# Optimization experiments

Hardware: AMD Instinct MI355X
Metric: run time of the kernel (lower is better)

The kernel has to match this reference:

```python
import jax, jax.numpy as jnp
import numpy as np

SIGMA = 0.01        # config['fscore_sigma']
FSCORE_W = 0.1      # config['fscore_weight']
TASK_W = 1.0        # config['task_weight']
DOMAIN_W = 0.1      # config['domain_weight']


def setup_inputs() -> dict:
    key = jax.random.key(0)
    ks = jax.random.split(key, 11)
    B, N, M, F = 8, 4096, 4096, 512
    H1, H2, D = 256, 128, 6
    return {
        "pred_pc": jax.random.normal(ks[0], (B, N, 3), jnp.float32),
        "target_pc": jax.random.normal(ks[1], (B, M, 3), jnp.float32),
        "domain_features": jax.random.normal(ks[2], (B, F), jnp.float32),
        "dataset_weights": jax.random.uniform(ks[3], (B,), jnp.float32, 0.9, 1.2),
        "W1": jax.random.normal(ks[4], (F, H1), jnp.float32) * 0.02,
        "b1": jnp.zeros((H1,), jnp.float32),
        "W2": jax.random.normal(ks[5], (H1, H2), jnp.float32) * 0.02,
        "b2": jnp.zeros((H2,), jnp.float32),
        "W3": jax.random.normal(ks[6], (H2, D), jnp.float32) * 0.02,
        "b3": jnp.zeros((D,), jnp.float32),
        "domain_labels": jax.random.randint(ks[7], (B,), 0, D),
    }


def _chamfer_mins(pred, tgt):
    # pred: [B,N,3], tgt: [B,M,3] -> squared pairwise dists [B,N,M], then dual mins
    d = (jnp.sum(pred ** 2, axis=2)[:, :, None]
         + jnp.sum(tgt ** 2, axis=2)[:, None, :]
         - 2.0 * jnp.einsum('bnd,bmd->bnm', pred, tgt))
    return jnp.min(d, axis=2), jnp.min(d, axis=1)   # [B,N], [B,M]


def reference(pred_pc, target_pc, domain_features, dataset_weights,
              W1, b1, W2, b2, W3, b3, domain_labels):
    min_a, min_b = _chamfer_mins(pred_pc, target_pc)
    c = 2.0 * SIGMA * SIGMA
    soft_a = jnp.exp(-min_a / c)
    soft_b = jnp.exp(-min_b / c)

    # batch-level task loss (compute_reconstruction_loss on full batch)
    chamfer = jnp.mean(min_a) + jnp.mean(min_b)
    prec = jnp.mean(soft_a)
    rec = jnp.mean(soft_b)
    fscore = 2.0 * prec * rec / (prec + rec + 1e-8)
    task = chamfer + FSCORE_W * (1.0 - fscore)

    # per-sample dataset-weighted loss (vectorized form of the Python loop)
    ch_i = jnp.mean(min_a, axis=1) + jnp.mean(min_b, axis=1)
    p_i = jnp.mean(soft_a, axis=1)
    r_i = jnp.mean(soft_b, axis=1)
    f_i = 2.0 * p_i * r_i / (p_i + r_i + 1e-8)
    loss_i = ch_i + FSCORE_W * (1.0 - f_i)
    dataset_weighted = jnp.mean(dataset_weights * loss_i)

    # domain loss: GRL is identity in forward; classifier in eval mode (dropout off)
    h = jax.nn.relu(domain_features @ W1 + b1)
    h = jax.nn.relu(h @ W2 + b2)
    logits = h @ W3 + b3
    logp = jax.nn.log_softmax(logits, axis=-1)
    domain = -jnp.mean(jnp.take_along_axis(logp, domain_labels[:, None], axis=1))

    total = TASK_W * task + DOMAIN_W * domain + dataset_weighted
    return total
```

## Files before the change

kernel.cpp:

```cpp
#include <hip/hip_runtime.h>
#include <math.h>

#define B 8
#define NPTS 4096
#define QPT 8
#define THREADS 256

typedef float v2f __attribute__((ext_vector_type(2)));
typedef float v4f __attribute__((ext_vector_type(4)));

__device__ __forceinline__ float min3f(float a, float b, float c) {
  return fminf(fminf(a, b), c);
}

#if __has_builtin(__builtin_elementwise_fma)
__device__ __forceinline__ v2f fma2(v2f a, v2f b, v2f c) {
  return __builtin_elementwise_fma(a, b, c);
}
#else
__device__ __forceinline__ v2f fma2(v2f a, v2f b, v2f c) {
  v2f r; r.x = __builtin_fmaf(a.x, b.x, c.x); r.y = __builtin_fmaf(a.y, b.y, c.y);
  return r;
}
#endif

#define VLO(v) __builtin_shufflevector(v, v, 0, 1)
#define VHI(v) __builtin_shufflevector(v, v, 2, 3)


template<int S, int LOG2S>
__global__ __launch_bounds__(THREADS, 4) void k1_kernel(
    const float* __restrict__ pred, const float* __restrict__ targ,
    const float* __restrict__ x, const float* __restrict__ W1,
    float* __restrict__ partial, float* __restrict__ sums64,
    float* __restrict__ h1p) {
  constexpr int REFS = NPTS / S;
  const int tid = threadIdx.x;
  const int cid = blockIdx.x;

  __shared__ __align__(16) float sx[REFS];
  __shared__ __align__(16) float sy[REFS];
  __shared__ __align__(16) float sz[REFS];
  __shared__ __align__(16) float sw[REFS];
  __shared__ float xs[64];

  if (cid < 64) {
    if (cid == 0 && tid < 64) sums64[tid] = 0.f;
    int b = cid >> 3, kc = cid & 7;
    if (tid < 64) xs[tid] = x[b * 512 + kc * 64 + tid];
    __syncthreads();
    float acc = 0.f;
    const float* w = W1 + (size_t)(kc * 64) * 256 + tid;
#pragma unroll 8
    for (int k = 0; k < 64; ++k) acc = fmaf(xs[k], w[k * 256], acc);
    h1p[(b * 8 + kc) * 256 + tid] = acc;
  }

  int split  = cid & (S - 1);
  int qchunk = (cid >> LOG2S) & 1;
  int b      = (cid >> (LOG2S + 1)) & 7;
  int dir    = cid >> (LOG2S + 4);
  const float* qp = dir ? targ : pred;
  const float* rp = dir ? pred : targ;

  const float* rb = rp + ((size_t)b * NPTS + (size_t)split * REFS) * 3;
  for (int i = tid; i < REFS; i += THREADS) {
    float xx = rb[i * 3 + 0], yy = rb[i * 3 + 1], zz = rb[i * 3 + 2];
    sx[i] = xx; sy[i] = yy; sz[i] = zz;
    sw[i] = 0.5f * (xx * xx + yy * yy + zz * zz);
  }
  __syncthreads();

  const float* qb = qp + (size_t)b * NPTS * 3;
  int q0 = qchunk * (QPT * THREADS) + tid;
  float qx[QPT], qy[QPT], qz[QPT], vmin[QPT];
#pragma unroll
  for (int i = 0; i < QPT; ++i) {
    int q = q0 + i * THREADS;
    qx[i] = qb[q * 3 + 0];
    qy[i] = qb[q * 3 + 1];
    qz[i] = qb[q * 3 + 2];
    vmin[i] = 3.4e38f;
  }

  for (int j = 0; j < REFS; j += 8) {
    v4f xA = *(const v4f*)(sx + j), xB = *(const v4f*)(sx + j + 4);
    v4f yA = *(const v4f*)(sy + j), yB = *(const v4f*)(sy + j + 4);
    v4f zA = *(const v4f*)(sz + j), zB = *(const v4f*)(sz + j + 4);
    v4f wA = *(const v4f*)(sw + j), wB = *(const v4f*)(sw + j + 4);
    v2f x01 = VLO(xA), x23 = VHI(xA), x45 = VLO(xB), x67 = VHI(xB);
    v2f y01 = VLO(yA), y23 = VHI(yA), y45 = VLO(yB), y67 = VHI(yB);
    v2f z01 = VLO(zA), z23 = VHI(zA), z45 = VLO(zB), z67 = VHI(zB);
    v2f w01 = VLO(wA), w23 = VHI(wA), w45 = VLO(wB), w67 = VHI(wB);
#pragma unroll
    for (int i = 0; i < QPT; ++i) {
      v2f nx = {-qx[i], -qx[i]};
      v2f ny = {-qy[i], -qy[i]};
      v2f nz = {-qz[i], -qz[i]};
      v2f s01 = fma2(nx, x01, fma2(ny, y01, fma2(nz, z01, w01)));
      v2f s23 = fma2(nx, x23, fma2(ny, y23, fma2(nz, z23, w23)));
      v2f s45 = fma2(nx, x45, fma2(ny, y45, fma2(nz, z45, w45)));
      v2f s67 = fma2(nx, x67, fma2(ny, y67, fma2(nz, z67, w67)));
      float m0 = min3f(s01.x, s01.y, s23.x);
      float m1 = min3f(s23.y, s45.x, s45.y);
      float m2 = min3f(s67.x, s67.y, m0);
      vmin[i] = min3f(m1, m2, vmin[i]);
    }
  }

  size_t base = (((size_t)dir * B + b) * S + split) * NPTS;
#pragma unroll
  for (int i = 0; i < QPT; ++i) {
    float qn = fmaf(qx[i], qx[i], fmaf(qy[i], qy[i], qz[i] * qz[i]));
    partial[base + q0 + i * THREADS] = fmaf(2.f, vmin[i], qn);
  }
}

template<int S>
__global__ __launch_bounds__(THREADS) void k2_kernel(
    const float* __restrict__ partial, float* __restrict__ sums64,
    const float* __restrict__ h1p, const float* __restrict__ b1,
    const float* __restrict__ W2, const float* __restrict__ b2,
    const float* __restrict__ W3, const float* __restrict__ b3,
    const int* __restrict__ labels, const float* __restrict__ wgt,
    float* __restrict__ out) {
  const int id = blockIdx.x;
  const int tid = threadIdx.x;
  __shared__ float red[8];
  __shared__ bool is_last;

  int chunk = id & 15;
  int b   = (id >> 4) & 7;
  int dir = id >> 7;
  size_t pb = ((size_t)dir * B + b) * S * NPTS;
  int q = chunk * 256 + tid;

  float m = 3.4e38f;
#pragma unroll
  for (int s = 0; s < S; ++s)
    m = fminf(m, partial[pb + (size_t)s * NPTS + q]);
  float s_min = m;
  float s_soft = __expf(-5000.0f * m);

  for (int off = 32; off > 0; off >>= 1) {
    s_min  += __shfl_down(s_min,  off);
    s_soft += __shfl_down(s_soft, off);
  }
  int wave = tid >> 6, lane = tid & 63;
  if (lane == 0) { red[wave * 2] = s_min; red[wave * 2 + 1] = s_soft; }
  __syncthreads();
  if (tid == 0) {
    float a = 0.f, c = 0.f;
    for (int wv = 0; wv < 4; ++wv) { a += red[wv * 2]; c += red[wv * 2 + 1]; }
    atomicAdd(&sums64[(dir * B + b) * 2 + 0], a);
    atomicAdd(&sums64[(dir * B + b) * 2 + 1], c);
    __threadfence();
    unsigned t = atomicAdd((unsigned*)(sums64 + 32), 1u);
    is_last = (t == 255u);
  }
  __syncthreads();
  if (!is_last) return;
  __threadfence();

  __shared__ float h1s[8 * 256];
  __shared__ float h2s[8 * 128];
  __shared__ float lg[48];
  __shared__ float nlls[8];

  for (int i = tid; i < 2048; i += THREADS) {
    int bb = i >> 8, k = i & 255;
    float a = b1[k];
#pragma unroll
    for (int p = 0; p < 8; ++p) a += h1p[(bb * 8 + p) * 256 + k];
    h1s[i] = fmaxf(a, 0.f);
  }
  __syncthreads();
  for (int i = tid; i < 1024; i += THREADS) {
    int bb = i >> 7, jo = i & 127;
    float acc = b2[jo];
    const float* w2 = W2 + jo;
    const float* h1r = h1s + bb * 256;
#pragma unroll 8
    for (int k = 0; k < 256; ++k) acc = fmaf(h1r[k], w2[(size_t)k * 128], acc);
    h2s[i] = fmaxf(acc, 0.f);
  }
  __syncthreads();
  if (tid < 48) {
    int bb = tid / 6, d = tid % 6;
    float acc = b3[d];
#pragma unroll 8
    for (int k = 0; k < 128; ++k)
      acc = fmaf(h2s[bb * 128 + k], W3[k * 6 + d], acc);
    lg[tid] = acc;
  }
  __syncthreads();
  if (tid < 8) {
    int bb = tid;
    float mx = lg[bb * 6];
    for (int d = 1; d < 6; ++d) mx = fmaxf(mx, lg[bb * 6 + d]);
    float se = 0.f;
    for (int d = 0; d < 6; ++d) se += __expf(lg[bb * 6 + d] - mx);
    int lab = labels[bb];
    nlls[bb] = -(lg[bb * 6 + lab] - mx - __logf(se));
  }
  __syncthreads();
  if (tid == 0) {
    volatile const float* vs = (volatile const float*)sums64;
    float chamfer = 0.f, prec = 0.f, rec = 0.f, dsw = 0.f, dom = 0.f;
    for (int bb = 0; bb < B; ++bb) {
      float sa  = vs[(0 * B + bb) * 2 + 0];
      float ssa = vs[(0 * B + bb) * 2 + 1];
      float sb  = vs[(1 * B + bb) * 2 + 0];
      float ssb = vs[(1 * B + bb) * 2 + 1];
      float ma = sa / 4096.f, mb = sb / 4096.f;
      float p = ssa / 4096.f, r = ssb / 4096.f;
      chamfer += ma + mb;
      prec += p; rec += r;
      float f_i = 2.f * p * r / (p + r + 1e-8f);
      float loss_i = ma + mb + 0.1f * (1.f - f_i);
      dsw += wgt[bb] * loss_i;
      dom += nlls[bb];
    }
    chamfer *= (1.f / B); prec *= (1.f / B); rec *= (1.f / B);
    dsw *= (1.f / B); dom *= (1.f / B);
    float fscore = 2.f * prec * rec / (prec + rec + 1e-8f);
    float task = chamfer + 0.1f * (1.f - fscore);
    out[0] = 1.0f * task + 0.1f * dom + dsw;
  }
}

template<int S, int LOG2S>
static void run_pipeline(const float* pred, const float* targ, const float* x,
                         const float* wgt, const float* W1, const float* b1,
                         const float* W2, const float* b2, const float* W3,
                         const float* b3, const int* labels, float* out,
                         char* ws, hipStream_t stream) {
  float* partial = (float*)ws;
  float* sums64  = partial + (size_t)2 * B * S * NPTS;
  float* h1p     = sums64 + 64;

  hipLaunchKernelGGL((k1_kernel<S, LOG2S>), dim3(32 * S), dim3(THREADS),
                     0, stream, pred, targ, x, W1, partial, sums64, h1p);
  hipLaunchKernelGGL((k2_kernel<S>), dim3(256), dim3(THREADS), 0, stream,
                     partial, sums64, h1p, b1, W2, b2, W3, b3, labels, wgt,
                     out);
}

extern "C" void kernel_launch(void* const* d_in, const int* in_sizes, int n_in,
                              void* d_out, int out_size, void* d_ws, size_t ws_size,
                              hipStream_t stream) {
  const float* pred   = (const float*)d_in[0];
  const float* targ   = (const float*)d_in[1];
  const float* x      = (const float*)d_in[2];
  const float* wgt    = (const float*)d_in[3];
  const float* W1     = (const float*)d_in[4];
  const float* b1     = (const float*)d_in[5];
  const float* W2     = (const float*)d_in[6];
  const float* b2     = (const float*)d_in[7];
  const float* W3     = (const float*)d_in[8];
  const float* b3     = (const float*)d_in[9];
  const int*   labels = (const int*)d_in[10];
  float* out = (float*)d_out;
  char* ws = (char*)d_ws;

  auto need = [](int S) {
    return ((size_t)2 * B * S * NPTS + 64 + 64 * 256) * sizeof(float);
  };
  if (ws_size >= need(32))
    run_pipeline<32, 5>(pred, targ, x, wgt, W1, b1, W2, b2, W3, b3, labels,
                        out, ws, stream);
  else if (ws_size >= need(16))
    run_pipeline<16, 4>(pred, targ, x, wgt, W1, b1, W2, b2, W3, b3, labels,
                        out, ws, stream);
  else
    run_pipeline<8, 3>(pred, targ, x, wgt, W1, b1, W2, b2, W3, b3, labels,
                       out, ws, stream);
}
```

Before: 137.4 us.

## Halve queries per thread, XCD-aware block mapping, and parallelize domain MLP layer

```diff
diff --git a/kernel.cpp b/kernel.cpp
--- a/kernel.cpp
+++ b/kernel.cpp
@@ -3,7 +3,8 @@
 
 #define B 8
 #define NPTS 4096
-#define QPT 8
+#define QPT 4
+#define QC  4
 #define THREADS 256
 
 typedef float v2f __attribute__((ext_vector_type(2)));
@@ -36,7 +37,7 @@
     float* __restrict__ h1p) {
   constexpr int REFS = NPTS / S;
   const int tid = threadIdx.x;
-  const int cid = blockIdx.x;
+  const int bid = blockIdx.x;
 
   __shared__ __align__(16) float sx[REFS];
   __shared__ __align__(16) float sy[REFS];
@@ -44,9 +45,9 @@
   __shared__ __align__(16) float sw[REFS];
   __shared__ float xs[64];
 
-  if (cid < 64) {
-    if (cid == 0 && tid < 64) sums64[tid] = 0.f;
-    int b = cid >> 3, kc = cid & 7;
+  if (bid < 64) {
+    if (bid == 0 && tid < 64) sums64[tid] = 0.f;
+    int b = bid >> 3, kc = bid & 7;
     if (tid < 64) xs[tid] = x[b * 512 + kc * 64 + tid];
     __syncthreads();
     float acc = 0.f;
@@ -54,34 +55,48 @@
 #pragma unroll 8
     for (int k = 0; k < 64; ++k) acc = fmaf(xs[k], w[k * 256], acc);
     h1p[(b * 8 + kc) * 256 + tid] = acc;
-  }
-
-  int split  = cid & (S - 1);
-  int qchunk = (cid >> LOG2S) & 1;
-  int b      = (cid >> (LOG2S + 1)) & 7;
-  int dir    = cid >> (LOG2S + 4);
+    __syncthreads();
+  }
+
+  int xcd  = bid & 7;
+  int spl  = (bid >> 3) & (S - 1);
+  int cs   = bid >> (3 + LOG2S);
+  int gid  = cs * 8 + xcd;
+  int qc   = gid & (QC - 1);
+  int b    = (gid >> 2) & 7;
+  int dir  = gid >> 5;
   const float* qp = dir ? targ : pred;
   const float* rp = dir ? pred : targ;
 
-  const float* rb = rp + ((size_t)b * NPTS + (size_t)split * REFS) * 3;
-  for (int i = tid; i < REFS; i += THREADS) {
-    float xx = rb[i * 3 + 0], yy = rb[i * 3 + 1], zz = rb[i * 3 + 2];
-    sx[i] = xx; sy[i] = yy; sz[i] = zz;
-    sw[i] = 0.5f * (xx * xx + yy * yy + zz * zz);
-  }
-  __syncthreads();
-
   const float* qb = qp + (size_t)b * NPTS * 3;
-  int q0 = qchunk * (QPT * THREADS) + tid;
-  float qx[QPT], qy[QPT], qz[QPT], vmin[QPT];
+  int q0 = qc * (QPT * THREADS) + tid;
+  float qx[QPT], qy[QPT], qz[QPT];
 #pragma unroll
   for (int i = 0; i < QPT; ++i) {
     int q = q0 + i * THREADS;
     qx[i] = qb[q * 3 + 0];
     qy[i] = qb[q * 3 + 1];
     qz[i] = qb[q * 3 + 2];
+  }
+
+  const float* rb = rp + ((size_t)b * NPTS + (size_t)spl * REFS) * 3;
+  for (int i = tid; i < REFS; i += THREADS) {
+    float xx = rb[i * 3 + 0], yy = rb[i * 3 + 1], zz = rb[i * 3 + 2];
+    sx[i] = xx; sy[i] = yy; sz[i] = zz;
+    sw[i] = 0.5f * (xx * xx + yy * yy + zz * zz);
+  }
+
+  float qn[QPT], vmin[QPT];
+  v2f bx[QPT], by[QPT], bz[QPT];
+#pragma unroll
+  for (int i = 0; i < QPT; ++i) {
+    qn[i] = fmaf(qx[i], qx[i], fmaf(qy[i], qy[i], qz[i] * qz[i]));
+    bx[i] = (v2f){-qx[i], -qx[i]};
+    by[i] = (v2f){-qy[i], -qy[i]};
+    bz[i] = (v2f){-qz[i], -qz[i]};
     vmin[i] = 3.4e38f;
   }
+  __syncthreads();
 
   for (int j = 0; j < REFS; j += 8) {
     v4f xA = *(const v4f*)(sx + j), xB = *(const v4f*)(sx + j + 4);
@@ -94,13 +109,10 @@
     v2f w01 = VLO(wA), w23 = VHI(wA), w45 = VLO(wB), w67 = VHI(wB);
 #pragma unroll
     for (int i = 0; i < QPT; ++i) {
-      v2f nx = {-qx[i], -qx[i]};
-      v2f ny = {-qy[i], -qy[i]};
-      v2f nz = {-qz[i], -qz[i]};
-      v2f s01 = fma2(nx, x01, fma2(ny, y01, fma2(nz, z01, w01)));
-      v2f s23 = fma2(nx, x23, fma2(ny, y23, fma2(nz, z23, w23)));
-      v2f s45 = fma2(nx, x45, fma2(ny, y45, fma2(nz, z45, w45)));
-      v2f s67 = fma2(nx, x67, fma2(ny, y67, fma2(nz, z67, w67)));
+      v2f s01 = fma2(bx[i], x01, fma2(by[i], y01, fma2(bz[i], z01, w01)));
+      v2f s23 = fma2(bx[i], x23, fma2(by[i], y23, fma2(bz[i], z23, w23)));
+      v2f s45 = fma2(bx[i], x45, fma2(by[i], y45, fma2(bz[i], z45, w45)));
+      v2f s67 = fma2(bx[i], x67, fma2(by[i], y67, fma2(bz[i], z67, w67)));
       float m0 = min3f(s01.x, s01.y, s23.x);
       float m1 = min3f(s23.y, s45.x, s45.y);
       float m2 = min3f(s67.x, s67.y, m0);
@@ -108,12 +120,10 @@
     }
   }
 
-  size_t base = (((size_t)dir * B + b) * S + split) * NPTS;
-#pragma unroll
-  for (int i = 0; i < QPT; ++i) {
-    float qn = fmaf(qx[i], qx[i], fmaf(qy[i], qy[i], qz[i] * qz[i]));
-    partial[base + q0 + i * THREADS] = fmaf(2.f, vmin[i], qn);
-  }
+  size_t base = (((size_t)dir * B + b) * S + spl) * NPTS;
+#pragma unroll
+  for (int i = 0; i < QPT; ++i)
+    partial[base + q0 + i * THREADS] = fmaf(2.f, vmin[i], qn[i]);
 }
 
 template<int S>
@@ -124,65 +134,83 @@
     const float* __restrict__ W3, const float* __restrict__ b3,
     const int* __restrict__ labels, const float* __restrict__ wgt,
     float* __restrict__ out) {
+  constexpr int NBLK = 272;
   const int id = blockIdx.x;
   const int tid = threadIdx.x;
   __shared__ float red[8];
+  __shared__ float hs[128];
   __shared__ bool is_last;
 
-  int chunk = id & 15;
-  int b   = (id >> 4) & 7;
-  int dir = id >> 7;
-  size_t pb = ((size_t)dir * B + b) * S * NPTS;
-  int q = chunk * 256 + tid;
-
-  float m = 3.4e38f;
-#pragma unroll
-  for (int s = 0; s < S; ++s)
-    m = fminf(m, partial[pb + (size_t)s * NPTS + q]);
-  float s_min = m;
-  float s_soft = __expf(-5000.0f * m);
-
-  for (int off = 32; off > 0; off >>= 1) {
-    s_min  += __shfl_down(s_min,  off);
-    s_soft += __shfl_down(s_soft, off);
-  }
-  int wave = tid >> 6, lane = tid & 63;
-  if (lane == 0) { red[wave * 2] = s_min; red[wave * 2 + 1] = s_soft; }
+  if (id >= 256) {
+    int lid = id - 256;
+    int b = lid >> 1, half = lid & 1;
+    if (tid < 128) {
+      int k = half * 128 + tid;
+      float a = b1[k];
+#pragma unroll
+      for (int p = 0; p < 8; ++p) a += h1p[(b * 8 + p) * 256 + k];
+      hs[tid] = fmaxf(a, 0.f);
+    }
+    __syncthreads();
+    if (tid < 128) {
+      float acc = 0.f;
+      const float* w = W2 + (size_t)(half * 128) * 128 + tid;
+#pragma unroll 8
+      for (int k = 0; k < 128; ++k) acc = fmaf(hs[k], w[k * 128], acc);
+      float* h2p = sums64 + 64 + 64 * 256;
+      h2p[(b * 2 + half) * 128 + tid] = acc;
+    }
+  } else {
+    int chunk = id & 15;
+    int b   = (id >> 4) & 7;
+    int dir = id >> 7;
+    size_t pb = ((size_t)dir * B + b) * S * NPTS;
+    int q = chunk * 256 + tid;
+
+    float v[S];
+#pragma unroll
+    for (int s = 0; s < S; ++s)
+      v[s] = partial[pb + (size_t)s * NPTS + q];
+    float m = v[0];
+#pragma unroll
+    for (int s = 1; s < S; ++s) m = fminf(m, v[s]);
+    float s_min = m;
+    float s_soft = __expf(-5000.0f * m);
+
+    for (int off = 32; off > 0; off >>= 1) {
+      s_min  += __shfl_down(s_min,  off);
+      s_soft += __shfl_down(s_soft, off);
+    }
+    int wave = tid >> 6, lane = tid & 63;
+    if (lane == 0) { red[wave * 2] = s_min; red[wave * 2 + 1] = s_soft; }
+    __syncthreads();
+    if (tid == 0) {
+      float a = 0.f, c = 0.f;
+      for (int wv = 0; wv < 4; ++wv) { a += red[wv * 2]; c += red[wv * 2 + 1]; }
+      atomicAdd(&sums64[(dir * B + b) * 2 + 0], a);
+      atomicAdd(&sums64[(dir * B + b) * 2 + 1], c);
+    }
+  }
+
+  __threadfence();
   __syncthreads();
   if (tid == 0) {
-    float a = 0.f, c = 0.f;
-    for (int wv = 0; wv < 4; ++wv) { a += red[wv * 2]; c += red[wv * 2 + 1]; }
-    atomicAdd(&sums64[(dir * B + b) * 2 + 0], a);
-    atomicAdd(&sums64[(dir * B + b) * 2 + 1], c);
-    __threadfence();
     unsigned t = atomicAdd((unsigned*)(sums64 + 32), 1u);
-    is_last = (t == 255u);
+    is_last = (t == NBLK - 1);
   }
   __syncthreads();
   if (!is_last) return;
   __threadfence();
 
-  __shared__ float h1s[8 * 256];
   __shared__ float h2s[8 * 128];
   __shared__ float lg[48];
   __shared__ float nlls[8];
-
-  for (int i = tid; i < 2048; i += THREADS) {
-    int bb = i >> 8, k = i & 255;
-    float a = b1[k];
-#pragma unroll
-    for (int p = 0; p < 8; ++p) a += h1p[(bb * 8 + p) * 256 + k];
-    h1s[i] = fmaxf(a, 0.f);
-  }
-  __syncthreads();
+  volatile const float* vh2 = (volatile const float*)(sums64 + 64 + 64 * 256);
+
   for (int i = tid; i < 1024; i += THREADS) {
-    int bb = i >> 7, jo = i & 127;
-    float acc = b2[jo];
-    const float* w2 = W2 + jo;
-    const float* h1r = h1s + bb * 256;
-#pragma unroll 8
-    for (int k = 0; k < 256; ++k) acc = fmaf(h1r[k], w2[(size_t)k * 128], acc);
-    h2s[i] = fmaxf(acc, 0.f);
+    int bb = i >> 7, j = i & 127;
+    float a = b2[j] + vh2[(bb * 2 + 0) * 128 + j] + vh2[(bb * 2 + 1) * 128 + j];
+    h2s[i] = fmaxf(a, 0.f);
   }
   __syncthreads();
   if (tid < 48) {
@@ -239,9 +267,9 @@
   float* sums64  = partial + (size_t)2 * B * S * NPTS;
   float* h1p     = sums64 + 64;
 
-  hipLaunchKernelGGL((k1_kernel<S, LOG2S>), dim3(32 * S), dim3(THREADS),
+  hipLaunchKernelGGL((k1_kernel<S, LOG2S>), dim3(64 * S), dim3(THREADS),
                      0, stream, pred, targ, x, W1, partial, sums64, h1p);
-  hipLaunchKernelGGL((k2_kernel<S>), dim3(256), dim3(THREADS), 0, stream,
+  hipLaunchKernelGGL((k2_kernel<S>), dim3(272), dim3(THREADS), 0, stream,
                      partial, sums64, h1p, b1, W2, b2, W3, b3, labels, wgt,
                      out);
 }
@@ -264,7 +292,7 @@
   char* ws = (char*)d_ws;
 
   auto need = [](int S) {
-    return ((size_t)2 * B * S * NPTS + 64 + 64 * 256) * sizeof(float);
+    return ((size_t)2 * B * S * NPTS + 64 + 64 * 256 + 16 * 128) * sizeof(float);
   };
   if (ws_size >= need(32))
     run_pipeline<32, 5>(pred, targ, x, wgt, W1, b1, W2, b2, W3, b3, labels,
```

After: 133.4 us. 1.03x faster.

## Fuse chamfer reduction and domain MLP into one kernel with last-block counters

Applied to the files above, without the earlier changes.

```diff
diff --git a/kernel.cpp b/kernel.cpp
--- a/kernel.cpp
+++ b/kernel.cpp
@@ -3,76 +3,165 @@
 
 #define B 8
 #define NPTS 4096
+#define THREADS 256
 #define QPT 8
-#define THREADS 256
-
-typedef float v2f __attribute__((ext_vector_type(2)));
-typedef float v4f __attribute__((ext_vector_type(4)));
+#define NGRP 32
+#define CTRL_BYTES 264
+
 
 __device__ __forceinline__ float min3f(float a, float b, float c) {
   return fminf(fminf(a, b), c);
 }
 
-#if __has_builtin(__builtin_elementwise_fma)
-__device__ __forceinline__ v2f fma2(v2f a, v2f b, v2f c) {
-  return __builtin_elementwise_fma(a, b, c);
-}
-#else
-__device__ __forceinline__ v2f fma2(v2f a, v2f b, v2f c) {
-  v2f r; r.x = __builtin_fmaf(a.x, b.x, c.x); r.y = __builtin_fmaf(a.y, b.y, c.y);
-  return r;
-}
-#endif
-
-#define VLO(v) __builtin_shufflevector(v, v, 0, 1)
-#define VHI(v) __builtin_shufflevector(v, v, 2, 3)
-
+__device__ void final_combine(const float* sums, const float* nlls,
+                              const float* __restrict__ wgt,
+                              float* __restrict__ out) {
+  volatile const float* vs = sums;
+  volatile const float* vn = nlls;
+  float chamfer = 0.f, prec = 0.f, rec = 0.f, dsw = 0.f, dom = 0.f;
+  for (int bb = 0; bb < B; ++bb) {
+    float sa  = vs[(0 * B + bb) * 2 + 0];
+    float ssa = vs[(0 * B + bb) * 2 + 1];
+    float sb  = vs[(1 * B + bb) * 2 + 0];
+    float ssb = vs[(1 * B + bb) * 2 + 1];
+    float ma = sa / 4096.f, mb = sb / 4096.f;
+    float p = ssa / 4096.f, r = ssb / 4096.f;
+    chamfer += ma + mb;
+    prec += p; rec += r;
+    float f_i = 2.f * p * r / (p + r + 1e-8f);
+    float loss_i = ma + mb + 0.1f * (1.f - f_i);
+    dsw += wgt[bb] * loss_i;
+    dom += vn[bb];
+  }
+  chamfer *= (1.f / B); prec *= (1.f / B); rec *= (1.f / B);
+  dsw *= (1.f / B); dom *= (1.f / B);
+  float fscore = 2.f * prec * rec / (prec + rec + 1e-8f);
+  float task = chamfer + 0.1f * (1.f - fscore);
+  out[0] = 1.0f * task + 0.1f * dom + dsw;
+}
 
 template<int S, int LOG2S>
-__global__ __launch_bounds__(THREADS, 4) void k1_kernel(
+__global__ __launch_bounds__(THREADS, 4) void fused(
     const float* __restrict__ pred, const float* __restrict__ targ,
     const float* __restrict__ x, const float* __restrict__ W1,
-    float* __restrict__ partial, float* __restrict__ sums64,
-    float* __restrict__ h1p) {
+    const float* __restrict__ b1, const float* __restrict__ W2,
+    const float* __restrict__ b2, const float* __restrict__ W3,
+    const float* __restrict__ b3, const int* __restrict__ labels,
+    const float* __restrict__ wgt, float* __restrict__ partial,
+    float* __restrict__ ctrl, float* __restrict__ out) {
   constexpr int REFS = NPTS / S;
   const int tid = threadIdx.x;
-  const int cid = blockIdx.x;
-
-  __shared__ __align__(16) float sx[REFS];
-  __shared__ __align__(16) float sy[REFS];
-  __shared__ __align__(16) float sz[REFS];
-  __shared__ __align__(16) float sw[REFS];
-  __shared__ float xs[64];
-
-  if (cid < 64) {
-    if (cid == 0 && tid < 64) sums64[tid] = 0.f;
-    int b = cid >> 3, kc = cid & 7;
-    if (tid < 64) xs[tid] = x[b * 512 + kc * 64 + tid];
-    __syncthreads();
+  const int bid = blockIdx.x;
+
+  float* sums = ctrl;
+  unsigned* gcnt    = (unsigned*)(ctrl + 32);
+  unsigned* mlp_cnt = (unsigned*)(ctrl + 64);
+  unsigned* fin_cnt = (unsigned*)(ctrl + 65);
+  float* nlls_g = ctrl + 66;
+  float* h1buf  = ctrl + 80;
+
+  __shared__ float4 refs[REFS];
+  __shared__ float red[8];
+  __shared__ unsigned sh_t;
+
+  if (bid >= NGRP * S) {
+    int mid = bid - NGRP * S;
+    int mb = mid >> 2, jc = (mid & 3) << 6;
+    __shared__ float xs[512];
+    __shared__ float ph[256];
+    xs[tid]       = x[mb * 512 + tid];
+    xs[256 + tid] = x[mb * 512 + 256 + tid];
+    __syncthreads();
+    int kq = tid >> 6, jj = tid & 63, j = jc + jj;
     float acc = 0.f;
-    const float* w = W1 + (size_t)(kc * 64) * 256 + tid;
+    const float* w1 = W1 + (size_t)(kq * 128) * 256 + j;
 #pragma unroll 8
-    for (int k = 0; k < 64; ++k) acc = fmaf(xs[k], w[k * 256], acc);
-    h1p[(b * 8 + kc) * 256 + tid] = acc;
-  }
-
-  int split  = cid & (S - 1);
-  int qchunk = (cid >> LOG2S) & 1;
-  int b      = (cid >> (LOG2S + 1)) & 7;
-  int dir    = cid >> (LOG2S + 4);
+    for (int k = 0; k < 128; ++k)
+      acc = fmaf(xs[kq * 128 + k], w1[(size_t)k * 256], acc);
+    ph[jj * 4 + kq] = acc;
+    __syncthreads();
+    if (tid < 64) {
+      float a = b1[jc + tid] + ph[tid * 4 + 0] + ph[tid * 4 + 1]
+              + ph[tid * 4 + 2] + ph[tid * 4 + 3];
+      h1buf[mb * 256 + jc + tid] = fmaxf(a, 0.f);
+    }
+    __threadfence();
+    __syncthreads();
+    if (tid == 0) sh_t = atomicAdd(mlp_cnt, 1u);
+    __syncthreads();
+    if (sh_t != 31u) return;
+    __threadfence();
+    __shared__ float h1s[2048];
+    __shared__ float h2s[1024];
+    __shared__ float lg[48];
+    __shared__ float nl[8];
+    for (int i = tid; i < 2048; i += THREADS)
+      h1s[i] = ((volatile const float*)h1buf)[i];
+    __syncthreads();
+    {
+      int jo = tid & 127, hb = tid >> 7;
+      float a0 = b2[jo], a1 = a0, a2 = a0, a3 = a0;
+      const float* w2 = W2 + jo;
+      for (int k = 0; k < 256; ++k) {
+        float w = w2[(size_t)k * 128];
+        a0 = fmaf(h1s[(0 + hb) * 256 + k], w, a0);
+        a1 = fmaf(h1s[(2 + hb) * 256 + k], w, a1);
+        a2 = fmaf(h1s[(4 + hb) * 256 + k], w, a2);
+        a3 = fmaf(h1s[(6 + hb) * 256 + k], w, a3);
+      }
+      h2s[(0 + hb) * 128 + jo] = fmaxf(a0, 0.f);
+      h2s[(2 + hb) * 128 + jo] = fmaxf(a1, 0.f);
+      h2s[(4 + hb) * 128 + jo] = fmaxf(a2, 0.f);
+      h2s[(6 + hb) * 128 + jo] = fmaxf(a3, 0.f);
+    }
+    __syncthreads();
+    if (tid < 48) {
+      int bb = tid / 6, d = tid % 6;
+      float acc3 = b3[d];
+#pragma unroll 8
+      for (int k = 0; k < 128; ++k)
+        acc3 = fmaf(h2s[bb * 128 + k], W3[k * 6 + d], acc3);
+      lg[tid] = acc3;
+    }
+    __syncthreads();
+    if (tid < 8) {
+      int bb = tid;
+      float mx = lg[bb * 6];
+      for (int d = 1; d < 6; ++d) mx = fmaxf(mx, lg[bb * 6 + d]);
+      float se = 0.f;
+      for (int d = 0; d < 6; ++d) se += __expf(lg[bb * 6 + d] - mx);
+      int lab = labels[bb];
+      nl[bb] = -(lg[bb * 6 + lab] - mx - __logf(se));
+    }
+    __syncthreads();
+    if (tid < 8) nlls_g[tid] = nl[tid];
+    __threadfence();
+    __syncthreads();
+    if (tid == 0) sh_t = atomicAdd(fin_cnt, 1u);
+    __syncthreads();
+    if (sh_t == NGRP && tid == 0) final_combine(sums, nlls_g, wgt, out);
+    return;
+  }
+
+  int xcd = bid & 7;
+  int spl = (bid >> 3) & (S - 1);
+  int cs  = bid >> (3 + LOG2S);
+  int g   = cs * 8 + xcd;
+  int qc  = g & 1;
+  int b   = (g >> 1) & 7;
+  int dir = g >> 4;
   const float* qp = dir ? targ : pred;
   const float* rp = dir ? pred : targ;
 
-  const float* rb = rp + ((size_t)b * NPTS + (size_t)split * REFS) * 3;
+  const float* rb = rp + ((size_t)b * NPTS + (size_t)spl * REFS) * 3;
   for (int i = tid; i < REFS; i += THREADS) {
     float xx = rb[i * 3 + 0], yy = rb[i * 3 + 1], zz = rb[i * 3 + 2];
-    sx[i] = xx; sy[i] = yy; sz[i] = zz;
-    sw[i] = 0.5f * (xx * xx + yy * yy + zz * zz);
+    refs[i] = make_float4(xx, yy, zz, 0.5f * (xx * xx + yy * yy + zz * zz));
   }
   __syncthreads();
 
   const float* qb = qp + (size_t)b * NPTS * 3;
-  int q0 = qchunk * (QPT * THREADS) + tid;
+  int q0 = qc * (QPT * THREADS) + tid;
   float qx[QPT], qy[QPT], qz[QPT], vmin[QPT];
 #pragma unroll
   for (int i = 0; i < QPT; ++i) {
@@ -83,149 +172,74 @@
     vmin[i] = 3.4e38f;
   }
 
-  for (int j = 0; j < REFS; j += 8) {
-    v4f xA = *(const v4f*)(sx + j), xB = *(const v4f*)(sx + j + 4);
-    v4f yA = *(const v4f*)(sy + j), yB = *(const v4f*)(sy + j + 4);
-    v4f zA = *(const v4f*)(sz + j), zB = *(const v4f*)(sz + j + 4);
-    v4f wA = *(const v4f*)(sw + j), wB = *(const v4f*)(sw + j + 4);
-    v2f x01 = VLO(xA), x23 = VHI(xA), x45 = VLO(xB), x67 = VHI(xB);
-    v2f y01 = VLO(yA), y23 = VHI(yA), y45 = VLO(yB), y67 = VHI(yB);
-    v2f z01 = VLO(zA), z23 = VHI(zA), z45 = VLO(zB), z67 = VHI(zB);
-    v2f w01 = VLO(wA), w23 = VHI(wA), w45 = VLO(wB), w67 = VHI(wB);
+  for (int jr = 0; jr < REFS; jr += 8) {
+    float4 t[8];
+#pragma unroll
+    for (int u = 0; u < 8; ++u) t[u] = refs[jr + u];
 #pragma unroll
     for (int i = 0; i < QPT; ++i) {
-      v2f nx = {-qx[i], -qx[i]};
-      v2f ny = {-qy[i], -qy[i]};
-      v2f nz = {-qz[i], -qz[i]};
-      v2f s01 = fma2(nx, x01, fma2(ny, y01, fma2(nz, z01, w01)));
-      v2f s23 = fma2(nx, x23, fma2(ny, y23, fma2(nz, z23, w23)));
-      v2f s45 = fma2(nx, x45, fma2(ny, y45, fma2(nz, z45, w45)));
-      v2f s67 = fma2(nx, x67, fma2(ny, y67, fma2(nz, z67, w67)));
-      float m0 = min3f(s01.x, s01.y, s23.x);
-      float m1 = min3f(s23.y, s45.x, s45.y);
-      float m2 = min3f(s67.x, s67.y, m0);
+      float s[8];
+#pragma unroll
+      for (int u = 0; u < 8; ++u)
+        s[u] = fmaf(-qx[i], t[u].x,
+               fmaf(-qy[i], t[u].y, fmaf(-qz[i], t[u].z, t[u].w)));
+      float m0 = min3f(s[0], s[1], s[2]);
+      float m1 = min3f(s[3], s[4], s[5]);
+      float m2 = min3f(s[6], s[7], m0);
       vmin[i] = min3f(m1, m2, vmin[i]);
     }
   }
 
-  size_t base = (((size_t)dir * B + b) * S + split) * NPTS;
+  size_t base = (((size_t)dir * B + b) * S + spl) * NPTS;
 #pragma unroll
   for (int i = 0; i < QPT; ++i) {
     float qn = fmaf(qx[i], qx[i], fmaf(qy[i], qy[i], qz[i] * qz[i]));
     partial[base + q0 + i * THREADS] = fmaf(2.f, vmin[i], qn);
   }
-}
-
-template<int S>
-__global__ __launch_bounds__(THREADS) void k2_kernel(
-    const float* __restrict__ partial, float* __restrict__ sums64,
-    const float* __restrict__ h1p, const float* __restrict__ b1,
-    const float* __restrict__ W2, const float* __restrict__ b2,
-    const float* __restrict__ W3, const float* __restrict__ b3,
-    const int* __restrict__ labels, const float* __restrict__ wgt,
-    float* __restrict__ out) {
-  const int id = blockIdx.x;
-  const int tid = threadIdx.x;
-  __shared__ float red[8];
-  __shared__ bool is_last;
-
-  int chunk = id & 15;
-  int b   = (id >> 4) & 7;
-  int dir = id >> 7;
-  size_t pb = ((size_t)dir * B + b) * S * NPTS;
-  int q = chunk * 256 + tid;
-
-  float m = 3.4e38f;
-#pragma unroll
-  for (int s = 0; s < S; ++s)
-    m = fminf(m, partial[pb + (size_t)s * NPTS + q]);
-  float s_min = m;
-  float s_soft = __expf(-5000.0f * m);
-
-  for (int off = 32; off > 0; off >>= 1) {
-    s_min  += __shfl_down(s_min,  off);
-    s_soft += __shfl_down(s_soft, off);
-  }
-  int wave = tid >> 6, lane = tid & 63;
-  if (lane == 0) { red[wave * 2] = s_min; red[wave * 2 + 1] = s_soft; }
+
+  __threadfence();
   __syncthreads();
-  if (tid == 0) {
-    float a = 0.f, c = 0.f;
-    for (int wv = 0; wv < 4; ++wv) { a += red[wv * 2]; c += red[wv * 2 + 1]; }
-    atomicAdd(&sums64[(dir * B + b) * 2 + 0], a);
-    atomicAdd(&sums64[(dir * B + b) * 2 + 1], c);
-    __threadfence();
-    unsigned t = atomicAdd((unsigned*)(sums64 + 32), 1u);
-    is_last = (t == 255u);
-  }
+  if (tid == 0) sh_t = atomicAdd(&gcnt[g], 1u);
   __syncthreads();
-  if (!is_last) return;
+  if (sh_t != (unsigned)(S - 1)) return;
+
   __threadfence();
-
-  __shared__ float h1s[8 * 256];
-  __shared__ float h2s[8 * 128];
-  __shared__ float lg[48];
-  __shared__ float nlls[8];
-
-  for (int i = tid; i < 2048; i += THREADS) {
-    int bb = i >> 8, k = i & 255;
-    float a = b1[k];
-#pragma unroll
-    for (int p = 0; p < 8; ++p) a += h1p[(bb * 8 + p) * 256 + k];
-    h1s[i] = fmaxf(a, 0.f);
-  }
-  __syncthreads();
-  for (int i = tid; i < 1024; i += THREADS) {
-    int bb = i >> 7, jo = i & 127;
-    float acc = b2[jo];
-    const float* w2 = W2 + jo;
-    const float* h1r = h1s + bb * 256;
-#pragma unroll 8
-    for (int k = 0; k < 256; ++k) acc = fmaf(h1r[k], w2[(size_t)k * 128], acc);
-    h2s[i] = fmaxf(acc, 0.f);
-  }
-  __syncthreads();
-  if (tid < 48) {
-    int bb = tid / 6, d = tid % 6;
-    float acc = b3[d];
-#pragma unroll 8
-    for (int k = 0; k < 128; ++k)
-      acc = fmaf(h2s[bb * 128 + k], W3[k * 6 + d], acc);
-    lg[tid] = acc;
-  }
-  __syncthreads();
-  if (tid < 8) {
-    int bb = tid;
-    float mx = lg[bb * 6];
-    for (int d = 1; d < 6; ++d) mx = fmaxf(mx, lg[bb * 6 + d]);
-    float se = 0.f;
-    for (int d = 0; d < 6; ++d) se += __expf(lg[bb * 6 + d] - mx);
-    int lab = labels[bb];
-    nlls[bb] = -(lg[bb * 6 + lab] - mx - __logf(se));
-  }
-  __syncthreads();
-  if (tid == 0) {
-    volatile const float* vs = (volatile const float*)sums64;
-    float chamfer = 0.f, prec = 0.f, rec = 0.f, dsw = 0.f, dom = 0.f;
-    for (int bb = 0; bb < B; ++bb) {
-      float sa  = vs[(0 * B + bb) * 2 + 0];
-      float ssa = vs[(0 * B + bb) * 2 + 1];
-      float sb  = vs[(1 * B + bb) * 2 + 0];
-      float ssb = vs[(1 * B + bb) * 2 + 1];
-      float ma = sa / 4096.f, mb = sb / 4096.f;
-      float p = ssa / 4096.f, r = ssb / 4096.f;
-      chamfer += ma + mb;
-      prec += p; rec += r;
-      float f_i = 2.f * p * r / (p + r + 1e-8f);
-      float loss_i = ma + mb + 0.1f * (1.f - f_i);
-      dsw += wgt[bb] * loss_i;
-      dom += nlls[bb];
-    }
-    chamfer *= (1.f / B); prec *= (1.f / B); rec *= (1.f / B);
-    dsw *= (1.f / B); dom *= (1.f / B);
-    float fscore = 2.f * prec * rec / (prec + rec + 1e-8f);
-    float task = chamfer + 0.1f * (1.f - fscore);
-    out[0] = 1.0f * task + 0.1f * dom + dsw;
+  {
+    const volatile float* vp = (const volatile float*)partial;
+    size_t pb = ((size_t)dir * B + b) * S * NPTS;
+    float s_min = 0.f, s_soft = 0.f;
+    for (int i = 0; i < QPT; ++i) {
+      int q = q0 + i * THREADS;
+      float v[S];
+#pragma unroll
+      for (int s = 0; s < S; ++s)
+        v[s] = vp[pb + (size_t)s * NPTS + q];
+      float m = v[0];
+#pragma unroll
+      for (int s = 1; s < S; ++s) m = fminf(m, v[s]);
+      s_min += m;
+      s_soft += __expf(-5000.0f * m);
+    }
+    for (int off = 32; off > 0; off >>= 1) {
+      s_min  += __shfl_down(s_min,  off);
+      s_soft += __shfl_down(s_soft, off);
+    }
+    int wave = tid >> 6, lane = tid & 63;
+    if (lane == 0) { red[wave * 2] = s_min; red[wave * 2 + 1] = s_soft; }
+    __syncthreads();
+    if (tid == 0) {
+      float a = 0.f, c = 0.f;
+      for (int wv = 0; wv < 4; ++wv) { a += red[wv * 2]; c += red[wv * 2 + 1]; }
+      atomicAdd(&sums[(dir * B + b) * 2 + 0], a);
+      atomicAdd(&sums[(dir * B + b) * 2 + 1], c);
+      __threadfence();
+      sh_t = atomicAdd(fin_cnt, 1u);
+    }
+    __syncthreads();
+    if (sh_t == NGRP) {
+      __threadfence();
+      if (tid == 0) final_combine(sums, nlls_g, wgt, out);
+    }
   }
 }
 
@@ -236,14 +250,12 @@
                          const float* b3, const int* labels, float* out,
                          char* ws, hipStream_t stream) {
   float* partial = (float*)ws;
-  float* sums64  = partial + (size_t)2 * B * S * NPTS;
-  float* h1p     = sums64 + 64;
-
-  hipLaunchKernelGGL((k1_kernel<S, LOG2S>), dim3(32 * S), dim3(THREADS),
-                     0, stream, pred, targ, x, W1, partial, sums64, h1p);
-  hipLaunchKernelGGL((k2_kernel<S>), dim3(256), dim3(THREADS), 0, stream,
-                     partial, sums64, h1p, b1, W2, b2, W3, b3, labels, wgt,
-                     out);
+  float* ctrl    = partial + (size_t)2 * B * S * NPTS;
+
+  hipMemsetAsync(ctrl, 0, CTRL_BYTES, stream);
+  hipLaunchKernelGGL((fused<S, LOG2S>), dim3(NGRP * S + 32), dim3(THREADS),
+                     0, stream, pred, targ, x, W1, b1, W2, b2, W3, b3,
+                     labels, wgt, partial, ctrl, out);
 }
 
 extern "C" void kernel_launch(void* const* d_in, const int* in_sizes, int n_in,
@@ -264,7 +276,7 @@
   char* ws = (char*)d_ws;
 
   auto need = [](int S) {
-    return ((size_t)2 * B * S * NPTS + 64 + 64 * 256) * sizeof(float);
+    return ((size_t)2 * B * S * NPTS + 80 + 2048) * sizeof(float);
   };
   if (ws_size >= need(32))
     run_pipeline<32, 5>(pred, targ, x, wgt, W1, b1, W2, b2, W3, b3, labels,
```

Result: slower. 258.4 us (+88.1%).
